# Performance work log

Hardware: AMD Instinct MI355X
Metric: run time of the kernel (lower is better)

Reference implementation:

```python
import jax, jax.numpy as jnp
import numpy as np

GAMMA = 9.6
BETA = 0.83
LAMDA = 10.0
EPS = 1e-12

B, D, C = 1024, 512, 10000


def _l2norm(x):
    # torch F.normalize: x / max(||x||_2, eps)
    n = jnp.sqrt(jnp.sum(x * x, axis=1, keepdims=True))
    return x / jnp.maximum(n, EPS)


def setup_inputs() -> dict:
    key = jax.random.key(0)
    k1, k2, k3, k4 = jax.random.split(key, 4)
    inp = jax.random.normal(k1, (B, D), dtype=jnp.float32)
    # xavier-uniform-like init for the classifier weight
    limit = float(np.sqrt(6.0 / (C + D)))
    weight = jax.random.uniform(k2, (C, D), dtype=jnp.float32, minval=-limit, maxval=limit)
    class_weight = jax.random.uniform(k3, (C,), dtype=jnp.float32)  # per-class margins in [0,1)
    label = jax.random.randint(k4, (B,), 0, C, dtype=jnp.int32)
    return {"input": inp, "weight": weight, "class_weight": class_weight, "label": label}


def reference(input, weight, class_weight, label):
    x = _l2norm(input)            # [B, D]
    w = _l2norm(weight)           # [C, D]
    fea = x @ w.T                 # [B, C] cosine logits

    # sp_i = fea[i, label_i]; logit_{ij} = sn_ij - sp_i + beta * m_j  (j != label_i)
    sp = jnp.take_along_axis(fea, label[:, None], axis=1)           # [B, 1]
    logits = GAMMA * (fea - sp + BETA * class_weight[None, :])      # [B, C]
    pos_mask = label[:, None] == jnp.arange(C, dtype=label.dtype)[None, :]
    logits = jnp.where(pos_mask, -jnp.inf, logits)                  # drop positive column
    lse = jax.scipy.special.logsumexp(logits, axis=1)               # [B]
    loss = jax.nn.softplus(lse)                                     # [B]

    # inter-class similarity penalty
    score = jnp.clip(w @ w.T, -1.0, 1.0)                            # [C, C]
    score = score * (1.0 - jnp.eye(C, dtype=score.dtype))           # zero diagonal
    s = jnp.max(score[label], axis=1)                               # [B]
    loss_w = jax.nn.softplus(jnp.mean(s) + 0.5)

    loss = loss + LAMDA * loss_w
    return fea, jnp.mean(loss)
```

## Files before the change

### kernel.cpp

```cpp
#include <hip/hip_runtime.h>
#include <math.h>

#define GAMMA 9.6f
#define BETA  0.83f
#define LAMDA 10.0f
#define B_ 1024
#define D_ 512
#define C_ 10000

#define WS_XB   0
#define WS_WB   1048576
#define WS_SU   11288576
#define WS_SUM  11292672

typedef __attribute__((ext_vector_type(8))) short short8;
typedef __attribute__((ext_vector_type(4))) float floatx4;

__device__ __forceinline__ unsigned enc_f(float f) {
    unsigned i = __float_as_uint(f);
    return (i & 0x80000000u) ? ~i : (i | 0x80000000u);
}
__device__ __forceinline__ float dec_f(unsigned u) {
    return (u & 0x80000000u) ? __uint_as_float(u ^ 0x80000000u)
                             : __uint_as_float(~u);
}
__device__ __forceinline__ float softplus_f(float x) {
    return (x > 30.f) ? x : log1pf(expf(x));
}
__device__ __forceinline__ unsigned short f2bf_rne(float f) {
    unsigned u = __float_as_uint(f);
    u += 0x7FFFu + ((u >> 16) & 1u);
    return (unsigned short)(u >> 16);
}

__global__ __launch_bounds__(128) void normcvt_kernel(
    const float* __restrict__ input, const float* __restrict__ weight,
    unsigned short* __restrict__ xb, unsigned short* __restrict__ wb,
    unsigned* __restrict__ s_u, float* __restrict__ sum_loss) {
    int row = blockIdx.x;
    int tid = threadIdx.x;
    if (row < B_ && tid == 0) s_u[row] = 0u;
    if (row == 0 && tid == 1) *sum_loss = 0.f;

    const float* src = (row < B_) ? (input + (size_t)row * D_)
                                  : (weight + (size_t)(row - B_) * D_);
    float4 v = *(const float4*)(src + tid * 4);
    float ss = v.x * v.x + v.y * v.y + v.z * v.z + v.w * v.w;
    #pragma unroll
    for (int o = 32; o > 0; o >>= 1) ss += __shfl_xor(ss, o, 64);
    __shared__ float red[2];
    if ((tid & 63) == 0) red[tid >> 6] = ss;
    __syncthreads();
    float inv = 1.0f / fmaxf(sqrtf(red[0] + red[1]), 1e-12f);
    unsigned short* dst = (row < B_) ? (xb + (size_t)row * D_)
                                     : (wb + (size_t)(row - B_) * D_);
    ushort4 o4;
    o4.x = f2bf_rne(v.x * inv);
    o4.y = f2bf_rne(v.y * inv);
    o4.z = f2bf_rne(v.z * inv);
    o4.w = f2bf_rne(v.w * inv);
    *(ushort4*)(dst + tid * 4) = o4;
}

#define BM 128
#define BN 128
#define BK 32
#define NTILE_M 16
#define NTILE_N 79
#define NWG (NTILE_M * NTILE_N)

__global__ __launch_bounds__(256) void mfma_gemm_kernel(
    const unsigned short* __restrict__ xb, const unsigned short* __restrict__ wb,
    const int* __restrict__ label,
    float* __restrict__ fea, unsigned* __restrict__ s_u) {
    __shared__ __align__(16) unsigned short As[2][BM * BK];
    __shared__ __align__(16) unsigned short Bs[2][BM * BK];
    __shared__ int lbl[BM];

    const int tid = threadIdx.x;
    const int orig = (blockIdx.x & 7) * (NWG / 8) + (blockIdx.x >> 3);
    const int m0 = (orig & 15) * BM;
    const int n0 = (orig >> 4) * BN;
    const bool feaTile = (m0 < B_);

    const int arow = tid >> 2;
    const int kc8 = (tid & 3) * 8;
    const unsigned short* asrc[2];
    const unsigned short* bsrc[2];
    #pragma unroll
    for (int q = 0; q < 2; q++) {
        int rm = m0 + arow + q * 64;
        const unsigned short* ab;
        if (rm < B_) ab = xb + (size_t)rm * D_;
        else         ab = wb + (size_t)label[rm - B_] * D_;
        asrc[q] = ab + kc8;
        int rn = n0 + arow + q * 64;
        if (rn >= C_) rn = C_ - 1;
        bsrc[q] = wb + (size_t)rn * D_ + kc8;
    }
    if (!feaTile && tid < BM) lbl[tid] = label[m0 - B_ + tid];

    const int lane = tid & 63;
    const int wv = tid >> 6;
    const int wr = (wv >> 1) * 64;
    const int wc = (wv & 1) * 64;
    const int l15 = lane & 15;
    const int hi = lane >> 4;

    floatx4 acc[4][4];
    #pragma unroll
    for (int i = 0; i < 4; i++)
        #pragma unroll
        for (int j = 0; j < 4; j++)
            acc[i][j] = (floatx4){0.f, 0.f, 0.f, 0.f};

#define STAGE(buf, kt)                                                         \
    {                                                                          \
        _Pragma("unroll")                                                      \
        for (int q = 0; q < 2; q++) {                                          \
            __builtin_amdgcn_global_load_lds(                                  \
                (const __attribute__((address_space(1))) void*)(asrc[q] + (kt)),\
                (__attribute__((address_space(3))) void*)((char*)&As[buf][0] + tid * 16 + q * 4096), \
                16, 0, 0);                                                     \
            __builtin_amdgcn_global_load_lds(                                  \
                (const __attribute__((address_space(1))) void*)(bsrc[q] + (kt)),\
                (__attribute__((address_space(3))) void*)((char*)&Bs[buf][0] + tid * 16 + q * 4096), \
                16, 0, 0);                                                     \
        }                                                                      \
    }

    STAGE(0, 0);
    __syncthreads();

    int cur = 0;
    for (int t = 0; t < D_ / BK; ++t) {
        int ktn = (t + 1) * BK;
        if (ktn < D_) STAGE(cur ^ 1, ktn);
        short8 a[4], b[4];
        #pragma unroll
        for (int i = 0; i < 4; i++)
            a[i] = *(const short8*)&As[cur][(wr + i * 16 + l15) * BK + hi * 8];
        #pragma unroll
        for (int j = 0; j < 4; j++)
            b[j] = *(const short8*)&Bs[cur][(wc + j * 16 + l15) * BK + hi * 8];
        #pragma unroll
        for (int i = 0; i < 4; i++)
            #pragma unroll
            for (int j = 0; j < 4; j++)
                acc[i][j] = __builtin_amdgcn_mfma_f32_16x16x32_bf16(
                    a[i], b[j], acc[i][j], 0, 0, 0);
        __syncthreads();
        cur ^= 1;
    }

    if (feaTile) {
        #pragma unroll
        for (int i = 0; i < 4; i++) {
            int m = m0 + wr + i * 16 + hi * 4;
            #pragma unroll
            for (int j = 0; j < 4; j++) {
                int n = n0 + wc + j * 16 + l15;
                if (n < C_) {
                    float* dst = fea + (size_t)m * C_ + n;
                    #pragma unroll
                    for (int r = 0; r < 4; r++)
                        dst[(size_t)r * C_] = acc[i][j][r];
                }
            }
        }
    } else {
        #pragma unroll
        for (int i = 0; i < 4; i++) {
            #pragma unroll
            for (int r = 0; r < 4; r++) {
                int row = wr + i * 16 + hi * 4 + r;
                int l = lbl[row];
                float vmax = -2.f;
                #pragma unroll
                for (int j = 0; j < 4; j++) {
                    int n = n0 + wc + j * 16 + l15;
                    float v = fminf(fmaxf(acc[i][j][r], -1.f), 1.f);
                    if (n == l) v = 0.f;
                    if (n < C_) vmax = fmaxf(vmax, v);
                }
                #pragma unroll
                for (int o = 8; o > 0; o >>= 1)
                    vmax = fmaxf(vmax, __shfl_xor(vmax, o, 64));
                if (l15 == 0) atomicMax(s_u + (m0 - B_ + row), enc_f(vmax));
            }
        }
    }
}

__global__ __launch_bounds__(256) void row_lse_kernel(
    const float* __restrict__ fea, const float* __restrict__ cw,
    const int* __restrict__ label, float* __restrict__ sum_loss) {
    int row = blockIdx.x;
    int tid = threadIdx.x;
    const float* fr = fea + (size_t)row * C_;
    int l = label[row];
    float m = -1e30f, s = 0.f;
    for (int t = tid; t < C_ / 4; t += 256) {
        float4 f = *(const float4*)(fr + t * 4);
        float4 c = *(const float4*)(cw + t * 4);
        float vals[4] = { f.x + BETA * c.x, f.y + BETA * c.y,
                          f.z + BETA * c.z, f.w + BETA * c.w };
        int j0 = t * 4;
        #pragma unroll
        for (int e = 0; e < 4; e++) {
            if (j0 + e == l) continue;
            float logit = GAMMA * vals[e];
            if (logit <= m) s += expf(logit - m);
            else { s = s * expf(m - logit) + 1.f; m = logit; }
        }
    }
    #pragma unroll
    for (int o = 32; o > 0; o >>= 1) {
        float om = __shfl_xor(m, o, 64);
        float os = __shfl_xor(s, o, 64);
        float nm = fmaxf(m, om);
        s = s * expf(m - nm) + os * expf(om - nm);
        m = nm;
    }
    __shared__ float red_m[4], red_s[4];
    if ((tid & 63) == 0) { red_m[tid >> 6] = m; red_s[tid >> 6] = s; }
    __syncthreads();
    if (tid == 0) {
        float M = red_m[0], S = red_s[0];
        #pragma unroll
        for (int wv = 1; wv < 4; wv++) {
            float om = red_m[wv], os = red_s[wv];
            float nm = fmaxf(M, om);
            S = S * expf(M - nm) + os * expf(om - nm);
            M = nm;
        }
        float sp = fr[l];
        float lse = M + logf(S) - GAMMA * sp;
        atomicAdd(sum_loss, softplus_f(lse));
    }
}

__global__ __launch_bounds__(1024) void final_kernel(
    const unsigned* __restrict__ s_u, const float* __restrict__ sum_loss,
    float* __restrict__ out_loss) {
    int tid = threadIdx.x;
    float s = dec_f(s_u[tid]);
    #pragma unroll
    for (int o = 32; o > 0; o >>= 1) s += __shfl_xor(s, o, 64);
    __shared__ float red[16];
    if ((tid & 63) == 0) red[tid >> 6] = s;
    __syncthreads();
    if (tid == 0) {
        float tot = 0.f;
        #pragma unroll
        for (int wv = 0; wv < 16; wv++) tot += red[wv];
        float loss_w = softplus_f(tot / (float)B_ + 0.5f);
        *out_loss = *sum_loss / (float)B_ + LAMDA * loss_w;
    }
}

extern "C" void kernel_launch(void* const* d_in, const int* in_sizes, int n_in,
                              void* d_out, int out_size, void* d_ws, size_t ws_size,
                              hipStream_t stream) {
    const float* input  = (const float*)d_in[0];
    const float* weight = (const float*)d_in[1];
    const float* cw     = (const float*)d_in[2];
    const int*   label  = (const int*)d_in[3];
    float* out = (float*)d_out;

    char* ws = (char*)d_ws;
    unsigned short* xb = (unsigned short*)(ws + WS_XB);
    unsigned short* wb = (unsigned short*)(ws + WS_WB);
    unsigned* s_u      = (unsigned*)(ws + WS_SU);
    float*    sum_loss = (float*)(ws + WS_SUM);

    normcvt_kernel<<<B_ + C_, 128, 0, stream>>>(input, weight, xb, wb, s_u, sum_loss);

    mfma_gemm_kernel<<<NWG, 256, 0, stream>>>(xb, wb, label, out, s_u);

    row_lse_kernel<<<B_, 256, 0, stream>>>(out, cw, label, sum_loss);
    final_kernel<<<1, 1024, 0, stream>>>(s_u, sum_loss, out + (size_t)B_ * C_);
}
```

Baseline: 81.33 us.

## Triple-buffer GEMM LDS staging with explicit vmcnt waits and raw barriers

Moves the MFMA GEMM main loop from double to triple buffering, issuing three K-slices of global-to-LDS loads up front and refilling each buffer after it is consumed. Full __syncthreads are replaced by explicit s_waitcnt vmcnt counts plus s_barrier, with sched_barrier fences and s_setprio raised around the MFMA block. The aim is to keep more loads in flight and hide memory latency. The shared label array is dropped in favour of reading labels from global memory in the epilogue. Costs are 50% more LDS per workgroup, which may reduce occupancy, and correctness now depends on the hand-counted vmcnt values.

```diff
diff --git a/kernel.cpp b/kernel.cpp
--- a/kernel.cpp
+++ b/kernel.cpp
@@ -65,6 +65,7 @@
 #define BM 128
 #define BN 128
 #define BK 32
+#define NSTEP (D_ / BK)
 #define NTILE_M 16
 #define NTILE_N 79
 #define NWG (NTILE_M * NTILE_N)
@@ -73,9 +74,8 @@
     const unsigned short* __restrict__ xb, const unsigned short* __restrict__ wb,
     const int* __restrict__ label,
     float* __restrict__ fea, unsigned* __restrict__ s_u) {
-    __shared__ __align__(16) unsigned short As[2][BM * BK];
-    __shared__ __align__(16) unsigned short Bs[2][BM * BK];
-    __shared__ int lbl[BM];
+    __shared__ __align__(16) unsigned short As[3][BM * BK];
+    __shared__ __align__(16) unsigned short Bs[3][BM * BK];
 
     const int tid = threadIdx.x;
     const int orig = (blockIdx.x & 7) * (NWG / 8) + (blockIdx.x >> 3);
@@ -98,7 +98,6 @@
         if (rn >= C_) rn = C_ - 1;
         bsrc[q] = wb + (size_t)rn * D_ + kc8;
     }
-    if (!feaTile && tid < BM) lbl[tid] = label[m0 - B_ + tid];
 
     const int lane = tid & 63;
     const int wv = tid >> 6;
@@ -130,27 +129,37 @@
     }
 
     STAGE(0, 0);
-    __syncthreads();
-
-    int cur = 0;
-    for (int t = 0; t < D_ / BK; ++t) {
-        int ktn = (t + 1) * BK;
-        if (ktn < D_) STAGE(cur ^ 1, ktn);
+    STAGE(1, BK);
+    STAGE(2, 2 * BK);
+
+    #pragma unroll
+    for (int t = 0; t < NSTEP; ++t) {
+        if (t <= NSTEP - 3)      asm volatile("s_waitcnt vmcnt(8)" ::: "memory");
+        else if (t == NSTEP - 2) asm volatile("s_waitcnt vmcnt(4)" ::: "memory");
+        else                     asm volatile("s_waitcnt vmcnt(0)" ::: "memory");
+        __builtin_amdgcn_s_barrier();
+        __builtin_amdgcn_sched_barrier(0);
+
+        const int buf = t % 3;
         short8 a[4], b[4];
         #pragma unroll
         for (int i = 0; i < 4; i++)
-            a[i] = *(const short8*)&As[cur][(wr + i * 16 + l15) * BK + hi * 8];
+            a[i] = *(const short8*)&As[buf][(wr + i * 16 + l15) * BK + hi * 8];
         #pragma unroll
         for (int j = 0; j < 4; j++)
-            b[j] = *(const short8*)&Bs[cur][(wc + j * 16 + l15) * BK + hi * 8];
+            b[j] = *(const short8*)&Bs[buf][(wc + j * 16 + l15) * BK + hi * 8];
+        __builtin_amdgcn_s_setprio(1);
         #pragma unroll
         for (int i = 0; i < 4; i++)
             #pragma unroll
             for (int j = 0; j < 4; j++)
                 acc[i][j] = __builtin_amdgcn_mfma_f32_16x16x32_bf16(
                     a[i], b[j], acc[i][j], 0, 0, 0);
-        __syncthreads();
-        cur ^= 1;
+        __builtin_amdgcn_s_setprio(0);
+
+        __builtin_amdgcn_s_barrier();
+        __builtin_amdgcn_sched_barrier(0);
+        if (t + 3 < NSTEP) STAGE(buf, (t + 3) * BK);
     }
 
     if (feaTile) {
@@ -174,7 +183,7 @@
             #pragma unroll
             for (int r = 0; r < 4; r++) {
                 int row = wr + i * 16 + hi * 4 + r;
-                int l = lbl[row];
+                int l = label[m0 - B_ + row];
                 float vmax = -2.f;
                 #pragma unroll
                 for (int j = 0; j < 4; j++) {
```

Result: no change. 80.82 us (-0.6%).

## Fuse logsumexp into GEMM epilogue with fixed-shift exp sums and wider N tiles

Applied to the files above, without the earlier changes.

Removes the separate row-wise logsumexp kernel. The GEMM epilogue now accumulates exp(gamma*(fea+beta*cw) - 20) per row via shuffles and atomicAdd, and records the positive logit. This uses a fixed shift instead of a running max, which is safe because cosine logits are bounded. The GEMM tile also grows to 128x256 with 512 threads, cutting the number of workgroups and reusing A tiles more. The cost is expf in the epilogue, more atomics, and a small change in float summation order.

```diff
diff --git a/kernel.cpp b/kernel.cpp
--- a/kernel.cpp
+++ b/kernel.cpp
@@ -7,11 +7,13 @@
 #define B_ 1024
 #define D_ 512
 #define C_ 10000
+#define M0_ 20.0f
 
 #define WS_XB   0
 #define WS_WB   1048576
 #define WS_SU   11288576
-#define WS_SUM  11292672
+#define WS_T    11292672
+#define WS_SP   11296768
 
 typedef __attribute__((ext_vector_type(8))) short short8;
 typedef __attribute__((ext_vector_type(4))) float floatx4;
@@ -36,11 +38,10 @@
 __global__ __launch_bounds__(128) void normcvt_kernel(
     const float* __restrict__ input, const float* __restrict__ weight,
     unsigned short* __restrict__ xb, unsigned short* __restrict__ wb,
-    unsigned* __restrict__ s_u, float* __restrict__ sum_loss) {
+    unsigned* __restrict__ s_u, float* __restrict__ T) {
     int row = blockIdx.x;
     int tid = threadIdx.x;
-    if (row < B_ && tid == 0) s_u[row] = 0u;
-    if (row == 0 && tid == 1) *sum_loss = 0.f;
+    if (row < B_ && tid == 0) { s_u[row] = 0u; T[row] = 0.f; }
 
     const float* src = (row < B_) ? (input + (size_t)row * D_)
                                   : (weight + (size_t)(row - B_) * D_);
@@ -63,19 +64,20 @@
 }
 
 #define BM 128
-#define BN 128
+#define BN 256
 #define BK 32
+#define NSTEP (D_ / BK)
 #define NTILE_M 16
-#define NTILE_N 79
+#define NTILE_N 40
 #define NWG (NTILE_M * NTILE_N)
 
-__global__ __launch_bounds__(256) void mfma_gemm_kernel(
+__global__ __launch_bounds__(512, 4) void mfma_gemm_kernel(
     const unsigned short* __restrict__ xb, const unsigned short* __restrict__ wb,
-    const int* __restrict__ label,
-    float* __restrict__ fea, unsigned* __restrict__ s_u) {
+    const int* __restrict__ label, const float* __restrict__ cw,
+    float* __restrict__ fea, unsigned* __restrict__ s_u,
+    float* __restrict__ T, float* __restrict__ sp) {
     __shared__ __align__(16) unsigned short As[2][BM * BK];
-    __shared__ __align__(16) unsigned short Bs[2][BM * BK];
-    __shared__ int lbl[BM];
+    __shared__ __align__(16) unsigned short Bs[2][BN * BK];
 
     const int tid = threadIdx.x;
     const int orig = (blockIdx.x & 7) * (NWG / 8) + (blockIdx.x >> 3);
@@ -83,27 +85,26 @@
     const int n0 = (orig >> 4) * BN;
     const bool feaTile = (m0 < B_);
 
-    const int arow = tid >> 2;
+    const int srow = tid >> 2;
     const int kc8 = (tid & 3) * 8;
-    const unsigned short* asrc[2];
+    const unsigned short* asrc;
+    {
+        int rm = m0 + srow;
+        if (rm < B_) asrc = xb + (size_t)rm * D_ + kc8;
+        else         asrc = wb + (size_t)label[rm - B_] * D_ + kc8;
+    }
     const unsigned short* bsrc[2];
     #pragma unroll
     for (int q = 0; q < 2; q++) {
-        int rm = m0 + arow + q * 64;
-        const unsigned short* ab;
-        if (rm < B_) ab = xb + (size_t)rm * D_;
-        else         ab = wb + (size_t)label[rm - B_] * D_;
-        asrc[q] = ab + kc8;
-        int rn = n0 + arow + q * 64;
+        int rn = n0 + srow + q * 128;
         if (rn >= C_) rn = C_ - 1;
         bsrc[q] = wb + (size_t)rn * D_ + kc8;
     }
-    if (!feaTile && tid < BM) lbl[tid] = label[m0 - B_ + tid];
 
     const int lane = tid & 63;
     const int wv = tid >> 6;
-    const int wr = (wv >> 1) * 64;
-    const int wc = (wv & 1) * 64;
+    const int wvr = (wv >> 2) * 64;
+    const int wvc = (wv & 3) * 64;
     const int l15 = lane & 15;
     const int hi = lane >> 4;
 
@@ -116,15 +117,15 @@
 
 #define STAGE(buf, kt)                                                         \
     {                                                                          \
+        __builtin_amdgcn_global_load_lds(                                      \
+            (const __attribute__((address_space(1))) void*)(asrc + (kt)),      \
+            (__attribute__((address_space(3))) void*)((char*)&As[buf][0] + tid * 16), \
+            16, 0, 0);                                                         \
         _Pragma("unroll")                                                      \
         for (int q = 0; q < 2; q++) {                                          \
             __builtin_amdgcn_global_load_lds(                                  \
-                (const __attribute__((address_space(1))) void*)(asrc[q] + (kt)),\
-                (__attribute__((address_space(3))) void*)((char*)&As[buf][0] + tid * 16 + q * 4096), \
-                16, 0, 0);                                                     \
-            __builtin_amdgcn_global_load_lds(                                  \
                 (const __attribute__((address_space(1))) void*)(bsrc[q] + (kt)),\
-                (__attribute__((address_space(3))) void*)((char*)&Bs[buf][0] + tid * 16 + q * 4096), \
+                (__attribute__((address_space(3))) void*)((char*)&Bs[buf][0] + tid * 16 + q * 8192), \
                 16, 0, 0);                                                     \
         }                                                                      \
     }
@@ -133,16 +134,16 @@
     __syncthreads();
 
     int cur = 0;
-    for (int t = 0; t < D_ / BK; ++t) {
+    for (int t = 0; t < NSTEP; ++t) {
         int ktn = (t + 1) * BK;
         if (ktn < D_) STAGE(cur ^ 1, ktn);
         short8 a[4], b[4];
         #pragma unroll
         for (int i = 0; i < 4; i++)
-            a[i] = *(const short8*)&As[cur][(wr + i * 16 + l15) * BK + hi * 8];
+            a[i] = *(const short8*)&As[cur][(wvr + i * 16 + l15) * BK + hi * 8];
         #pragma unroll
         for (int j = 0; j < 4; j++)
-            b[j] = *(const short8*)&Bs[cur][(wc + j * 16 + l15) * BK + hi * 8];
+            b[j] = *(const short8*)&Bs[cur][(wvc + j * 16 + l15) * BK + hi * 8];
         #pragma unroll
         for (int i = 0; i < 4; i++)
             #pragma unroll
@@ -154,31 +155,65 @@
     }
 
     if (feaTile) {
+        int lbl_ir[4][4];
+        #pragma unroll
+        for (int i = 0; i < 4; i++)
+            #pragma unroll
+            for (int r = 0; r < 4; r++)
+                lbl_ir[i][r] = label[m0 + wvr + i * 16 + hi * 4 + r];
+        float cwj[4];
+        #pragma unroll
+        for (int j = 0; j < 4; j++) {
+            int n = n0 + wvc + j * 16 + l15;
+            cwj[j] = (n < C_) ? cw[n] : 0.f;
+        }
+        float rs[4][4];
+        #pragma unroll
+        for (int i = 0; i < 4; i++)
+            #pragma unroll
+            for (int r = 0; r < 4; r++) rs[i][r] = 0.f;
+
         #pragma unroll
         for (int i = 0; i < 4; i++) {
-            int m = m0 + wr + i * 16 + hi * 4;
             #pragma unroll
             for (int j = 0; j < 4; j++) {
-                int n = n0 + wc + j * 16 + l15;
+                int n = n0 + wvc + j * 16 + l15;
                 if (n < C_) {
+                    int m = m0 + wvr + i * 16 + hi * 4;
                     float* dst = fea + (size_t)m * C_ + n;
                     #pragma unroll
-                    for (int r = 0; r < 4; r++)
-                        dst[(size_t)r * C_] = acc[i][j][r];
+                    for (int r = 0; r < 4; r++) {
+                        float v = acc[i][j][r];
+                        dst[(size_t)r * C_] = v;
+                        int l = lbl_ir[i][r];
+                        if (n == l) sp[m + r] = v;
+                        else rs[i][r] += expf(GAMMA * (v + BETA * cwj[j]) - M0_);
+                    }
                 }
             }
         }
+        #pragma unroll
+        for (int i = 0; i < 4; i++) {
+            #pragma unroll
+            for (int r = 0; r < 4; r++) {
+                float s = rs[i][r];
+                #pragma unroll
+                for (int o = 8; o > 0; o >>= 1) s += __shfl_xor(s, o, 64);
+                if (l15 == 0)
+                    atomicAdd(T + (m0 + wvr + i * 16 + hi * 4 + r), s);
+            }
+        }
     } else {
         #pragma unroll
         for (int i = 0; i < 4; i++) {
             #pragma unroll
             for (int r = 0; r < 4; r++) {
-                int row = wr + i * 16 + hi * 4 + r;
-                int l = lbl[row];
+                int row = m0 - B_ + wvr + i * 16 + hi * 4 + r;
+                int l = label[row];
                 float vmax = -2.f;
                 #pragma unroll
                 for (int j = 0; j < 4; j++) {
-                    int n = n0 + wc + j * 16 + l15;
+                    int n = n0 + wvc + j * 16 + l15;
                     float v = fminf(fmaxf(acc[i][j][r], -1.f), 1.f);
                     if (n == l) v = 0.f;
                     if (n < C_) vmax = fmaxf(vmax, v);
@@ -186,76 +221,33 @@
                 #pragma unroll
                 for (int o = 8; o > 0; o >>= 1)
                     vmax = fmaxf(vmax, __shfl_xor(vmax, o, 64));
-                if (l15 == 0) atomicMax(s_u + (m0 - B_ + row), enc_f(vmax));
+                if (l15 == 0) atomicMax(s_u + row, enc_f(vmax));
             }
         }
     }
 }
 
-__global__ __launch_bounds__(256) void row_lse_kernel(
-    const float* __restrict__ fea, const float* __restrict__ cw,
-    const int* __restrict__ label, float* __restrict__ sum_loss) {
-    int row = blockIdx.x;
+__global__ __launch_bounds__(1024) void final_kernel(
+    const unsigned* __restrict__ s_u, const float* __restrict__ T,
+    const float* __restrict__ sp, float* __restrict__ out_loss) {
     int tid = threadIdx.x;
-    const float* fr = fea + (size_t)row * C_;
-    int l = label[row];
-    float m = -1e30f, s = 0.f;
-    for (int t = tid; t < C_ / 4; t += 256) {
-        float4 f = *(const float4*)(fr + t * 4);
-        float4 c = *(const float4*)(cw + t * 4);
-        float vals[4] = { f.x + BETA * c.x, f.y + BETA * c.y,
-                          f.z + BETA * c.z, f.w + BETA * c.w };
-        int j0 = t * 4;
-        #pragma unroll
-        for (int e = 0; e < 4; e++) {
-            if (j0 + e == l) continue;
-            float logit = GAMMA * vals[e];
-            if (logit <= m) s += expf(logit - m);
-            else { s = s * expf(m - logit) + 1.f; m = logit; }
-        }
-    }
+    float lse = M0_ + logf(T[tid]) - GAMMA * sp[tid];
+    float lr = softplus_f(lse);
+    float sv = dec_f(s_u[tid]);
     #pragma unroll
     for (int o = 32; o > 0; o >>= 1) {
-        float om = __shfl_xor(m, o, 64);
-        float os = __shfl_xor(s, o, 64);
-        float nm = fmaxf(m, om);
-        s = s * expf(m - nm) + os * expf(om - nm);
-        m = nm;
-    }
-    __shared__ float red_m[4], red_s[4];
-    if ((tid & 63) == 0) { red_m[tid >> 6] = m; red_s[tid >> 6] = s; }
+        lr += __shfl_xor(lr, o, 64);
+        sv += __shfl_xor(sv, o, 64);
+    }
+    __shared__ float red_l[16], red_s[16];
+    if ((tid & 63) == 0) { red_l[tid >> 6] = lr; red_s[tid >> 6] = sv; }
     __syncthreads();
     if (tid == 0) {
-        float M = red_m[0], S = red_s[0];
-        #pragma unroll
-        for (int wv = 1; wv < 4; wv++) {
-            float om = red_m[wv], os = red_s[wv];
-            float nm = fmaxf(M, om);
-            S = S * expf(M - nm) + os * expf(om - nm);
-            M = nm;
-        }
-        float sp = fr[l];
-        float lse = M + logf(S) - GAMMA * sp;
-        atomicAdd(sum_loss, softplus_f(lse));
-    }
-}
-
-__global__ __launch_bounds__(1024) void final_kernel(
-    const unsigned* __restrict__ s_u, const float* __restrict__ sum_loss,
-    float* __restrict__ out_loss) {
-    int tid = threadIdx.x;
-    float s = dec_f(s_u[tid]);
-    #pragma unroll
-    for (int o = 32; o > 0; o >>= 1) s += __shfl_xor(s, o, 64);
-    __shared__ float red[16];
-    if ((tid & 63) == 0) red[tid >> 6] = s;
-    __syncthreads();
-    if (tid == 0) {
-        float tot = 0.f;
-        #pragma unroll
-        for (int wv = 0; wv < 16; wv++) tot += red[wv];
-        float loss_w = softplus_f(tot / (float)B_ + 0.5f);
-        *out_loss = *sum_loss / (float)B_ + LAMDA * loss_w;
+        float tl = 0.f, ts = 0.f;
+        #pragma unroll
+        for (int wv = 0; wv < 16; wv++) { tl += red_l[wv]; ts += red_s[wv]; }
+        float loss_w = softplus_f(ts / (float)B_ + 0.5f);
+        *out_loss = tl / (float)B_ + LAMDA * loss_w;
     }
 }
 
@@ -272,12 +264,12 @@
     unsigned short* xb = (unsigned short*)(ws + WS_XB);
     unsigned short* wb = (unsigned short*)(ws + WS_WB);
     unsigned* s_u      = (unsigned*)(ws + WS_SU);
-    float*    sum_loss = (float*)(ws + WS_SUM);
-
-    normcvt_kernel<<<B_ + C_, 128, 0, stream>>>(input, weight, xb, wb, s_u, sum_loss);
-
-    mfma_gemm_kernel<<<NWG, 256, 0, stream>>>(xb, wb, label, out, s_u);
-
-    row_lse_kernel<<<B_, 256, 0, stream>>>(out, cw, label, sum_loss);
-    final_kernel<<<1, 1024, 0, stream>>>(s_u, sum_loss, out + (size_t)B_ * C_);
-}
+    float*    T        = (float*)(ws + WS_T);
+    float*    sp       = (float*)(ws + WS_SP);
+
+    normcvt_kernel<<<B_ + C_, 128, 0, stream>>>(input, weight, xb, wb, s_u, T);
+
+    mfma_gemm_kernel<<<NWG, 512, 0, stream>>>(xb, wb, label, cw, out, s_u, T, sp);
+
+    final_kernel<<<1, 1024, 0, stream>>>(s_u, T, sp, out + (size_t)B_ * C_);
+}
```

New measurement: 71.10 us. -12.6%, faster.
